# Optimization experiments

Hardware: AMD Instinct MI355X
Metric: run time of the kernel (lower is better)

## Reference

```python
import jax, jax.numpy as jnp
import numpy as np

REEIG_EPS = 1e-4  # standard SPDNet ReEig rectification threshold


def _bimap(X, W):
    # X: [B, C, n, n] SPD, W: [C, n, m] semi-orthogonal -> W^T X W : [B, C, m, m]
    return jnp.einsum('cik,bcij,cjl->bckl', W, X, W)


def _reeig(X):
    # Eigen-rectification: clamp eigenvalues at REEIG_EPS, reconstruct.
    w, U = jnp.linalg.eigh(X)
    w = jnp.maximum(w, REEIG_EPS)
    return jnp.einsum('bcik,bck,bcjk->bcij', U, w, U)


def _logeig(X):
    # Matrix log via eigendecomposition (eigenvalues > 0 after ReEig).
    w, U = jnp.linalg.eigh(X)
    return jnp.einsum('bcik,bck,bcjk->bcij', U, jnp.log(w), U)


def setup_inputs() -> dict:
    key = jax.random.key(0)
    k_x, k_w1, k_w2, k_wl, k_bl = jax.random.split(key, 5)
    B, n1, n2, n_cls = 131072, 12, 11, 52
    # Build SPD inputs: A A^T / n + eps I
    A = jax.random.normal(k_x, (B, 1, n1, n1), dtype=jnp.float32)
    x = jnp.einsum('bcij,bckj->bcik', A, A) / n1 + 1e-3 * jnp.eye(n1, dtype=jnp.float32)
    # Stiefel (semi-orthogonal) BiMap weights, as in SPDNet
    Q1 = jnp.linalg.qr(jax.random.normal(k_w1, (n1, n1), dtype=jnp.float32))[0]
    w1 = Q1[None, :, :]                      # [1, 12, 12]
    Q2 = jnp.linalg.qr(jax.random.normal(k_w2, (n1, n1), dtype=jnp.float32))[0]
    w2 = Q2[:, :n2][None, :, :]              # [1, 12, 11]
    w_lin = jax.random.normal(k_wl, (n_cls, n2 * n2), dtype=jnp.float32) * (1.0 / np.sqrt(n2 * n2))
    b_lin = jnp.zeros((n_cls,), dtype=jnp.float32)
    return {"x": x, "w1": w1, "w2": w2, "w_lin": w_lin, "b_lin": b_lin}


def reference(x, w1, w2, w_lin, b_lin):
    h = _reeig(_bimap(x, w1))                # [B,1,12,12]
    h = _reeig(_bimap(h, w2))                # [B,1,11,11]
    h = _logeig(h).reshape(x.shape[0], -1)   # [B,121]
    return h @ w_lin.T + b_lin               # [B,52]
```

## Files before the change

kernel.cpp:

```cpp
#include <hip/hip_runtime.h>
#include <math.h>


#define NSWEEP 5

#define WS_V 0
#define WS_B 160
#define WS_W 256

__device__ __forceinline__ constexpr int UT(int i, int j) {
  return i * 11 - (i * (i - 1)) / 2 + (j - i);
}

template <int P, int Q>
__device__ __forceinline__ void csCompute(const float (&M)[66], float& c, float& s,
                                          float& t) {
  const float app = M[UT(P, P)], aqq = M[UT(Q, Q)], apq = M[UT(P, Q)];
  const float d2 = aqq - app;
  const float a2 = apq + apq;
  const float r = __builtin_amdgcn_sqrtf(
      __builtin_fmaf(d2, d2, __builtin_fmaf(a2, a2, 1e-60f)));
  const float den = d2 + __builtin_copysignf(r, d2);
  t = a2 * __builtin_amdgcn_rcpf(den);
  c = __builtin_amdgcn_rsqf(__builtin_fmaf(t, t, 1.0f));
  s = t * c;
}

template <int P, int Q>
__device__ __forceinline__ void applyRot(float (&M)[66], float (&U)[121], float c,
                                         float s, float t) {
  const float apq = M[UT(P, Q)];
#pragma unroll
  for (int k = 0; k < 11; ++k) {
    if (k == P || k == Q) continue;
    const int ikp = (k < P) ? UT(k, P) : UT(P, k);
    const int ikq = (k < Q) ? UT(k, Q) : UT(Q, k);
    const float akp = M[ikp], akq = M[ikq];
    M[ikp] = __builtin_fmaf(c, akp, -s * akq);
    M[ikq] = __builtin_fmaf(s, akp, c * akq);
  }
  M[UT(P, P)] = __builtin_fmaf(-t, apq, M[UT(P, P)]);
  M[UT(Q, Q)] = __builtin_fmaf(t, apq, M[UT(Q, Q)]);
  M[UT(P, Q)] = 0.0f;
#pragma unroll
  for (int k = 0; k < 11; ++k) {
    const float ukp = U[k * 11 + P], ukq = U[k * 11 + Q];
    U[k * 11 + P] = __builtin_fmaf(c, ukp, -s * ukq);
    U[k * 11 + Q] = __builtin_fmaf(s, ukp, c * ukq);
  }
}

template <int R, int K>
struct PairRR {
  static constexpr int A0 = (R + K) % 11;
  static constexpr int B0 = (R + 11 - K) % 11;
  static constexpr int P = A0 < B0 ? A0 : B0;
  static constexpr int Q = A0 < B0 ? B0 : A0;
};

template <int R>
__device__ __forceinline__ void jround(float (&M)[66], float (&U)[121]) {
  float c1, s1, t1, c2, s2, t2, c3, s3, t3, c4, s4, t4, c5, s5, t5;
  csCompute<PairRR<R, 1>::P, PairRR<R, 1>::Q>(M, c1, s1, t1);
  csCompute<PairRR<R, 2>::P, PairRR<R, 2>::Q>(M, c2, s2, t2);
  csCompute<PairRR<R, 3>::P, PairRR<R, 3>::Q>(M, c3, s3, t3);
  csCompute<PairRR<R, 4>::P, PairRR<R, 4>::Q>(M, c4, s4, t4);
  csCompute<PairRR<R, 5>::P, PairRR<R, 5>::Q>(M, c5, s5, t5);
  applyRot<PairRR<R, 1>::P, PairRR<R, 1>::Q>(M, U, c1, s1, t1);
  applyRot<PairRR<R, 2>::P, PairRR<R, 2>::Q>(M, U, c2, s2, t2);
  applyRot<PairRR<R, 3>::P, PairRR<R, 3>::Q>(M, U, c3, s3, t3);
  applyRot<PairRR<R, 4>::P, PairRR<R, 4>::Q>(M, U, c4, s4, t4);
  applyRot<PairRR<R, 5>::P, PairRR<R, 5>::Q>(M, U, c5, s5, t5);
}

template <int R>
struct RoundSeq {
  static __device__ __forceinline__ void run(float (&M)[66], float (&U)[121]) {
    jround<R>(M, U);
    if constexpr (R < 10) RoundSeq<R + 1>::run(M, U);
  }
};

__global__ __launch_bounds__(256) void prep_kernel(
    const float* __restrict__ w1, const float* __restrict__ w2,
    const float* __restrict__ wlin, const float* __restrict__ blin,
    float* __restrict__ ws) {
  const int g = blockIdx.x * 256 + threadIdx.x;
  const int gs = gridDim.x * 256;
  for (int idx = g; idx < 144; idx += gs) {
    const int i = idx / 12, l = idx % 12;
    float acc = 0.f;
    if (l < 11) {
#pragma unroll
      for (int j = 0; j < 12; ++j) acc = __builtin_fmaf(w1[i * 12 + j], w2[j * 11 + l], acc);
    }
    ws[WS_V + idx] = acc;
  }
  for (int idx = g; idx < 52; idx += gs) ws[WS_B + idx] = blin[idx];
  for (int idx = g; idx < 52 * 68; idx += gs) {
    const int c = idx / 68, t = idx % 68;
    float v = 0.f;
    if (t < 66) {
      int i = 0, rem = t;
      while (rem >= 11 - i) { rem -= 11 - i; ++i; }
      const int j = i + rem;
      v = wlin[c * 121 + i * 11 + j];
      if (i != j) v += wlin[c * 121 + j * 11 + i];
    }
    ws[WS_W + idx] = v;
  }
}

__global__ __attribute__((amdgpu_flat_work_group_size(256, 256)))
__attribute__((amdgpu_waves_per_eu(1, 1)))
void manifold_kernel(const float* __restrict__ x, const float* __restrict__ ws,
                     float* __restrict__ out, int B) {
  __shared__ __align__(16) float sV[12 * 12];
  const int tid = threadIdx.x;
  if (tid < 36) {
    reinterpret_cast<float4*>(sV)[tid] =
        reinterpret_cast<const float4*>(ws + WS_V)[tid];
  }
  __syncthreads();

  const int b = blockIdx.x * 256 + tid;
  if (b >= B) return;

  float T[132];
#pragma unroll
  for (int e = 0; e < 132; ++e) T[e] = 0.f;
  const float4* xb4 = reinterpret_cast<const float4*>(x + (size_t)b * 144);
#pragma unroll 1
  for (int i = 0; i < 12; ++i) {
    const float4 a0 = xb4[i * 3 + 0], a1 = xb4[i * 3 + 1], a2 = xb4[i * 3 + 2];
    const float xr[12] = {a0.x, a0.y, a0.z, a0.w, a1.x, a1.y, a1.z, a1.w,
                          a2.x, a2.y, a2.z, a2.w};
    const float4 v0 = *reinterpret_cast<const float4*>(&sV[i * 12 + 0]);
    const float4 v1 = *reinterpret_cast<const float4*>(&sV[i * 12 + 4]);
    const float4 v2 = *reinterpret_cast<const float4*>(&sV[i * 12 + 8]);
    const float vr[11] = {v0.x, v0.y, v0.z, v0.w, v1.x, v1.y, v1.z, v1.w,
                          v2.x, v2.y, v2.z};
#pragma unroll
    for (int k = 0; k < 11; ++k)
#pragma unroll
      for (int j = 0; j < 12; ++j)
        T[k * 12 + j] = __builtin_fmaf(vr[k], xr[j], T[k * 12 + j]);
  }

  float M[66];
#pragma unroll
  for (int e = 0; e < 66; ++e) M[e] = 0.f;
#pragma unroll
  for (int j = 0; j < 12; ++j) {
    const float4 v0 = *reinterpret_cast<const float4*>(&sV[j * 12 + 0]);
    const float4 v1 = *reinterpret_cast<const float4*>(&sV[j * 12 + 4]);
    const float4 v2 = *reinterpret_cast<const float4*>(&sV[j * 12 + 8]);
    const float vr[11] = {v0.x, v0.y, v0.z, v0.w, v1.x, v1.y, v1.z, v1.w,
                          v2.x, v2.y, v2.z};
#pragma unroll
    for (int k = 0; k < 11; ++k) {
      const float tkj = T[k * 12 + j];
#pragma unroll
      for (int l = k; l < 11; ++l)
        M[UT(k, l)] = __builtin_fmaf(tkj, vr[l], M[UT(k, l)]);
    }
  }

  float U[121];
#pragma unroll
  for (int e = 0; e < 121; ++e) U[e] = 0.f;
#pragma unroll
  for (int d = 0; d < 11; ++d) U[d * 11 + d] = 1.f;
#pragma unroll 1
  for (int sweep = 0; sweep < NSWEEP; ++sweep) {
    RoundSeq<0>::run(M, U);
  }

  float lw[11];
#pragma unroll
  for (int k = 0; k < 11; ++k) lw[k] = __logf(fmaxf(M[UT(k, k)], 1e-4f));

  float L[66];
#pragma unroll
  for (int i = 0; i < 11; ++i) {
    float tk[11];
#pragma unroll
    for (int k = 0; k < 11; ++k) tk[k] = lw[k] * U[i * 11 + k];
#pragma unroll
    for (int j = i; j < 11; ++j) {
      float acc = 0.f;
#pragma unroll
      for (int k = 0; k < 11; ++k) acc = __builtin_fmaf(tk[k], U[j * 11 + k], acc);
      L[UT(i, j)] = acc;
    }
  }

  const float* __restrict__ wsym = ws + WS_W;
  const float* __restrict__ bl = ws + WS_B;
  float* ob = out + (size_t)b * 52;
#pragma unroll 1
  for (int c4 = 0; c4 < 13; ++c4) {
    float ov[4];
#pragma unroll
    for (int cc = 0; cc < 4; ++cc) {
      const int c = c4 * 4 + cc;
      const float* wr = wsym + c * 68;
      float a0 = 0.f, a1 = 0.f, a2 = 0.f, a3 = 0.f;
#pragma unroll
      for (int t = 0; t < 64; t += 4) {
        a0 = __builtin_fmaf(wr[t + 0], L[t + 0], a0);
        a1 = __builtin_fmaf(wr[t + 1], L[t + 1], a1);
        a2 = __builtin_fmaf(wr[t + 2], L[t + 2], a2);
        a3 = __builtin_fmaf(wr[t + 3], L[t + 3], a3);
      }
      a0 = __builtin_fmaf(wr[64], L[64], a0);
      a1 = __builtin_fmaf(wr[65], L[65], a1);
      ov[cc] = bl[c] + ((a0 + a1) + (a2 + a3));
    }
    float4 o;
    o.x = ov[0]; o.y = ov[1]; o.z = ov[2]; o.w = ov[3];
    reinterpret_cast<float4*>(ob)[c4] = o;
  }
}

extern "C" void kernel_launch(void* const* d_in, const int* in_sizes, int n_in,
                              void* d_out, int out_size, void* d_ws, size_t ws_size,
                              hipStream_t stream) {
  const float* x = (const float*)d_in[0];
  const float* w1 = (const float*)d_in[1];
  const float* w2 = (const float*)d_in[2];
  const float* wlin = (const float*)d_in[3];
  const float* blin = (const float*)d_in[4];
  float* out = (float*)d_out;
  float* ws = (float*)d_ws;
  const int B = in_sizes[0] / 144;
  hipLaunchKernelGGL(prep_kernel, dim3(8), dim3(256), 0, stream,
                     w1, w2, wlin, blin, ws);
  const int grid = (B + 255) / 256;
  hipLaunchKernelGGL(manifold_kernel, dim3(grid), dim3(256), 0, stream,
                     x, ws, out, B);
}
```

Measured before the change: 312.2 us.

## Restructure congruence transform to shrink register footprint and allow two waves per EU

```diff
diff --git a/kernel.cpp b/kernel.cpp
--- a/kernel.cpp
+++ b/kernel.cpp
@@ -112,7 +112,7 @@
 }
 
 __global__ __attribute__((amdgpu_flat_work_group_size(256, 256)))
-__attribute__((amdgpu_waves_per_eu(1, 1)))
+__attribute__((amdgpu_waves_per_eu(2)))
 void manifold_kernel(const float* __restrict__ x, const float* __restrict__ ws,
                      float* __restrict__ out, int B) {
   __shared__ __align__(16) float sV[12 * 12];
@@ -126,43 +126,53 @@
   const int b = blockIdx.x * 256 + tid;
   if (b >= B) return;
 
-  float T[132];
-#pragma unroll
-  for (int e = 0; e < 132; ++e) T[e] = 0.f;
+  float M[66];
+#pragma unroll
+  for (int e = 0; e < 66; ++e) M[e] = 0.f;
   const float4* xb4 = reinterpret_cast<const float4*>(x + (size_t)b * 144);
 #pragma unroll 1
-  for (int i = 0; i < 12; ++i) {
-    const float4 a0 = xb4[i * 3 + 0], a1 = xb4[i * 3 + 1], a2 = xb4[i * 3 + 2];
-    const float xr[12] = {a0.x, a0.y, a0.z, a0.w, a1.x, a1.y, a1.z, a1.w,
-                          a2.x, a2.y, a2.z, a2.w};
-    const float4 v0 = *reinterpret_cast<const float4*>(&sV[i * 12 + 0]);
-    const float4 v1 = *reinterpret_cast<const float4*>(&sV[i * 12 + 4]);
-    const float4 v2 = *reinterpret_cast<const float4*>(&sV[i * 12 + 8]);
-    const float vr[11] = {v0.x, v0.y, v0.z, v0.w, v1.x, v1.y, v1.z, v1.w,
-                          v2.x, v2.y, v2.z};
-#pragma unroll
-    for (int k = 0; k < 11; ++k)
-#pragma unroll
-      for (int j = 0; j < 12; ++j)
-        T[k * 12 + j] = __builtin_fmaf(vr[k], xr[j], T[k * 12 + j]);
-  }
-
-  float M[66];
-#pragma unroll
-  for (int e = 0; e < 66; ++e) M[e] = 0.f;
-#pragma unroll
-  for (int j = 0; j < 12; ++j) {
-    const float4 v0 = *reinterpret_cast<const float4*>(&sV[j * 12 + 0]);
-    const float4 v1 = *reinterpret_cast<const float4*>(&sV[j * 12 + 4]);
-    const float4 v2 = *reinterpret_cast<const float4*>(&sV[j * 12 + 8]);
-    const float vr[11] = {v0.x, v0.y, v0.z, v0.w, v1.x, v1.y, v1.z, v1.w,
-                          v2.x, v2.y, v2.z};
-#pragma unroll
-    for (int k = 0; k < 11; ++k) {
-      const float tkj = T[k * 12 + j];
-#pragma unroll
-      for (int l = k; l < 11; ++l)
-        M[UT(k, l)] = __builtin_fmaf(tkj, vr[l], M[UT(k, l)]);
+  for (int ib = 0; ib < 3; ++ib) {
+    float xr[4][12];
+#pragma unroll
+    for (int r = 0; r < 4; ++r) {
+      const float4 a0 = xb4[(ib * 4 + r) * 3 + 0];
+      const float4 a1 = xb4[(ib * 4 + r) * 3 + 1];
+      const float4 a2 = xb4[(ib * 4 + r) * 3 + 2];
+      xr[r][0] = a0.x; xr[r][1] = a0.y; xr[r][2] = a0.z; xr[r][3] = a0.w;
+      xr[r][4] = a1.x; xr[r][5] = a1.y; xr[r][6] = a1.z; xr[r][7] = a1.w;
+      xr[r][8] = a2.x; xr[r][9] = a2.y; xr[r][10] = a2.z; xr[r][11] = a2.w;
+    }
+    float w[4][11];
+#pragma unroll
+    for (int r = 0; r < 4; ++r)
+#pragma unroll
+      for (int l = 0; l < 11; ++l) w[r][l] = 0.f;
+#pragma unroll
+    for (int j = 0; j < 12; ++j) {
+      const float4 v0 = *reinterpret_cast<const float4*>(&sV[j * 12 + 0]);
+      const float4 v1 = *reinterpret_cast<const float4*>(&sV[j * 12 + 4]);
+      const float4 v2 = *reinterpret_cast<const float4*>(&sV[j * 12 + 8]);
+      const float vr[11] = {v0.x, v0.y, v0.z, v0.w, v1.x, v1.y, v1.z, v1.w,
+                            v2.x, v2.y, v2.z};
+#pragma unroll
+      for (int r = 0; r < 4; ++r)
+#pragma unroll
+        for (int l = 0; l < 11; ++l)
+          w[r][l] = __builtin_fmaf(xr[r][j], vr[l], w[r][l]);
+    }
+#pragma unroll
+    for (int r = 0; r < 4; ++r) {
+      const int i = ib * 4 + r;
+      const float4 u0 = *reinterpret_cast<const float4*>(&sV[i * 12 + 0]);
+      const float4 u1 = *reinterpret_cast<const float4*>(&sV[i * 12 + 4]);
+      const float4 u2 = *reinterpret_cast<const float4*>(&sV[i * 12 + 8]);
+      const float ui[11] = {u0.x, u0.y, u0.z, u0.w, u1.x, u1.y, u1.z, u1.w,
+                            u2.x, u2.y, u2.z};
+#pragma unroll
+      for (int k = 0; k < 11; ++k)
+#pragma unroll
+        for (int l = k; l < 11; ++l)
+          M[UT(k, l)] = __builtin_fmaf(ui[k], w[r][l], M[UT(k, l)]);
     }
   }
 
```

After: 871.0 us. 2.79x slower.
